# Optimization experiments

Hardware: AMD Instinct MI355X
Metric: run time of the kernel (lower is better)

## Reference

```python
import jax, jax.numpy as jnp
import numpy as np

B, H, W = 8, 256, 256
GH, GW = 32, 32          # orig_grid_shape, = img / 2^3 after three stride-2 convs
N_STEPS = 6              # masks_num: r_x_total=3, r_y_total=3, alternating dim_stride
C_FEAT = 64
N_MASK = 4               # 4 shifted supervoxel masks summed in setup
DN = ('NHWC', 'HWIO', 'NHWC')
# deconves_importances[r_x-1]; r_x sequence over steps = 1,1,2,2,3,3
LOSS_W = (0.1, 0.1, 0.5, 0.5, 1.0, 1.0)


def _conv(x, w, b, strides=(1, 1)):
    return jax.lax.conv_general_dilated(x, w, strides, 'SAME', dimension_numbers=DN) + b


def _trio(x, w, b, strides=(1, 1)):
    # Conv_trio: conv + channel norm + gelu
    y = _conv(x, w, b, strides)
    mu = jnp.mean(y, axis=-1, keepdims=True)
    var = jnp.var(y, axis=-1, keepdims=True)
    y = (y - mu) * jax.lax.rsqrt(var + 1e-6)
    return jax.nn.gelu(y)


def setup_inputs() -> dict:
    key = jax.random.key(0)
    ks = jax.random.split(key, 8)
    s = 0.05
    w1 = jax.random.normal(ks[0], (3, 3, 1, 16), jnp.float32) * s
    w2 = jax.random.normal(ks[1], (3, 3, 16, 16), jnp.float32) * s
    w3 = jax.random.normal(ks[2], (3, 3, 16, 32), jnp.float32) * s
    w4 = jax.random.normal(ks[3], (3, 3, 32, C_FEAT), jnp.float32) * s
    up_w = jax.random.normal(ks[4], (3, 3, C_FEAT, C_FEAT), jnp.float32) * s
    mask_w = jax.random.normal(ks[5], (3, 3, C_FEAT, N_MASK), jnp.float32) * s
    b1 = jnp.zeros((16,)); b2 = jnp.zeros((16,)); b3 = jnp.zeros((32,))
    b4 = jnp.zeros((C_FEAT,)); up_b = jnp.zeros((C_FEAT,)); mask_b = jnp.zeros((N_MASK,))
    # initial supervoxel masks: sum of 4 shifted checkerboards -> per-cell grid ids
    xs = jnp.arange(GH) % 2
    ys = jnp.arange(GW) % 2
    ids = (xs[:, None] + 2 * ys[None, :]).astype(jnp.float32)  # [GH,GW] in {0,1,2,3}
    masks0 = jnp.broadcast_to(ids[None, :, :, None], (B, GH, GW, 1))
    image = jax.random.normal(ks[6], (B, H, W, 1), jnp.float32)
    return {"image": image, "dynamic_cfg": 0,
            "w1": w1, "b1": b1, "w2": w2, "b2": b2, "w3": w3, "b3": b3,
            "w4": w4, "b4": b4, "up_w": up_w, "up_b": up_b,
            "mask_w": mask_w, "mask_b": mask_b, "masks0": masks0}


def reference(image, dynamic_cfg, w1, b1, w2, b2, w3, b3, w4, b4,
              up_w, up_b, mask_w, mask_b, masks0):
    # encoder: Conv_trio(16) -> (16,s2) -> (32,s2) -> (64,s2)
    x = _trio(image, w1, b1)
    x = _trio(x, w2, b2, (2, 2))
    x = _trio(x, w3, b3, (2, 2))
    deconv_multi = _trio(x, w4, b4, (2, 2))  # [B,32,32,64]
    masks = masks0
    losses = jnp.zeros((1,), image.dtype)
    offsets = jnp.arange(N_MASK, dtype=image.dtype)
    for i in range(N_STEPS):  # fixed, structurally distinct resolutions
        dim = i % 2  # alternating dim_stride as in r_x_r_y_dim_stride
        strides = (2, 1) if dim == 0 else (1, 2)
        deconv_multi = jax.nn.gelu(
            jax.lax.conv_transpose(deconv_multi, up_w, strides, 'SAME',
                                   dimension_numbers=DN) + up_b)
        probs = jax.nn.softmax(_conv(deconv_multi, mask_w, mask_b), axis=-1)  # [B,h,w,4]
        masks = jnp.repeat(masks, 2, axis=dim + 1)
        masks = masks + 0.25 * jnp.sum(probs * offsets, axis=-1, keepdims=True)
        h, w_ = deconv_multi.shape[1], deconv_multi.shape[2]
        img_ds = image.reshape(B, h, H // h, w_, W // w_, 1).mean(axis=(2, 4))
        recon = jnp.sum(probs * offsets, axis=-1, keepdims=True) / 3.0
        entropy = -jnp.sum(probs * jnp.log(probs + 1e-8), axis=-1)
        losses = losses + LOSS_W[i] * (jnp.mean(entropy) + jnp.mean((recon - img_ds) ** 2))
    return losses, masks
```

## Files before the change

### kernel.cpp

```cpp
#include <hip/hip_runtime.h>
#include <hip/hip_bf16.h>
#include <math.h>

typedef __hip_bfloat16 bf16;
typedef float f32x4 __attribute__((ext_vector_type(4)));
typedef __bf16 bf16x8 __attribute__((ext_vector_type(8)));

#define DEV __device__ __forceinline__

DEV float to_f(float v){ return v; }
DEV float to_f(bf16 v){ return __bfloat162float(v); }
DEV bf16 f2b(float v){ return __float2bfloat16(v); }
DEV unsigned short b2u(bf16 v){ return __builtin_bit_cast(unsigned short, v); }

DEV float gelu_f(float x){
  float z = 1.5957691216057308f*(x + 0.044715f*x*x*x);
  float e = __expf(-z);
  return x * __builtin_amdgcn_rcpf(1.0f + e);
}

DEV bf16x8 load_frag(const bf16* p, bool ok){
  uint4 u = make_uint4(0u,0u,0u,0u);
  if (ok) u = *(const uint4*)p;
  return __builtin_bit_cast(bf16x8, u);
}

DEV f32x4 mfma16(bf16x8 a, uint4 b, f32x4 c){
  return __builtin_amdgcn_mfma_f32_16x16x32_bf16(a, __builtin_bit_cast(bf16x8, b), c, 0, 0, 0);
}

DEV int swz8(int blk, int n){
  return (blk & 7) * (n >> 3) + (blk >> 3);
}

DEV void dma16(const void* g, void* l){
  __builtin_amdgcn_global_load_lds(
      (const __attribute__((address_space(1))) unsigned int*)g,
      (__attribute__((address_space(3))) unsigned int*)l,
      16, 0, 0);
}

#define NSLOT 64

template<typename TIN, int CIN, int COUT, int SUB, int STRIDE, int HI, int WI>
__global__ void trio_kernel(const TIN* __restrict__ in, const float* __restrict__ w,
                            const float* __restrict__ bias, bf16* __restrict__ out){
  constexpr int HO = HI/STRIDE, WO = WI/STRIDE;
  constexpr int CO_PER = COUT/SUB;
  int gtid = blockIdx.x*blockDim.x + threadIdx.x;
  int sub = gtid % SUB;
  int pix = gtid / SUB;
  int b = pix / (HO*WO); int rem = pix % (HO*WO);
  int y = rem / WO, x = rem % WO;

  float acc[CO_PER];
  #pragma unroll
  for (int j=0;j<CO_PER;j++) acc[j]=0.f;

  for (int ky=0;ky<3;ky++){
    int iy = (STRIDE==1) ? (y+ky-1) : (2*y+ky);
    if (iy<0 || iy>=HI) continue;
    for (int kx=0;kx<3;kx++){
      int ix = (STRIDE==1) ? (x+kx-1) : (2*x+kx);
      if (ix<0 || ix>=WI) continue;
      const TIN* ip = in + ((size_t)(b*HI+iy)*WI+ix)*CIN;
      const float* wp = w + ((ky*3+kx)*CIN)*COUT + sub*CO_PER;
      if constexpr (sizeof(TIN)==2 && (CIN%8)==0){
        #pragma unroll
        for (int v=0; v<CIN/8; v++){
          uint4 u = *(const uint4*)((const bf16*)ip + v*8);
          bf16x8 ch = __builtin_bit_cast(bf16x8, u);
          #pragma unroll
          for (int j=0;j<8;j++){
            float a = (float)ch[j];
            const float4* w4 = (const float4*)(wp + (size_t)(v*8+j)*COUT);
            #pragma unroll
            for (int q2=0;q2<CO_PER/4;q2++){
              float4 ww = w4[q2];
              acc[4*q2+0] += a*ww.x; acc[4*q2+1] += a*ww.y;
              acc[4*q2+2] += a*ww.z; acc[4*q2+3] += a*ww.w;
            }
          }
        }
      } else {
        #pragma unroll 4
        for (int ci=0; ci<CIN; ci++){
          float a = to_f(ip[ci]);
          const float4* w4 = (const float4*)(wp + (size_t)ci*COUT);
          #pragma unroll
          for (int j=0;j<CO_PER/4;j++){
            float4 ww = w4[j];
            acc[4*j+0] += a*ww.x; acc[4*j+1] += a*ww.y;
            acc[4*j+2] += a*ww.z; acc[4*j+3] += a*ww.w;
          }
        }
      }
    }
  }

  float s1=0.f, s2=0.f;
  #pragma unroll
  for (int j=0;j<CO_PER;j++){
    acc[j] += bias[sub*CO_PER+j];
    s1 += acc[j]; s2 += acc[j]*acc[j];
  }
  #pragma unroll
  for (int off=1; off<SUB; off<<=1){
    s1 += __shfl_xor(s1,off,64);
    s2 += __shfl_xor(s2,off,64);
  }
  float mu  = s1*(1.0f/COUT);
  float var = s2*(1.0f/COUT) - mu*mu;
  float sc  = rsqrtf(var + 1e-6f);

  bf16* op = out + (size_t)pix*COUT + sub*CO_PER;
  #pragma unroll
  for (int j=0;j<CO_PER;j++) op[j] = f2b(gelu_f((acc[j]-mu)*sc));
}

__global__ void repack_up(const float* __restrict__ w, bf16* __restrict__ bp){
  int v = blockIdx.x*256 + threadIdx.x;
  if (v >= 9*2*4*64*8) return;
  int j = v & 7; int lane = (v>>3)&63; int nt = (v>>9)&3; int c = (v>>11)&1; int tap = v>>12;
  int ci = c*32 + (lane>>4)*8 + j;
  int co = (lane&15)*4 + nt;
  bp[v] = f2b(w[(tap*64+ci)*64 + co]);
}

__global__ void repack_mask(const float* __restrict__ w, bf16* __restrict__ bp){
  int v = blockIdx.x*256 + threadIdx.x;
  if (v >= 9*2*64*8) return;
  int j = v & 7; int lane = (v>>3)&63; int c = (v>>9)&1; int tap = v>>10;
  int ci = c*32 + (lane>>4)*8 + j;
  int n = lane & 15;
  bp[v] = (n < 4) ? f2b(w[(tap*64+ci)*4 + n]) : f2b(0.0f);
}

template<int HI, int WI>
__global__ void upconv_dim0(const bf16* __restrict__ in, const bf16* __restrict__ bpack,
                            const float* __restrict__ upb, bf16* __restrict__ out){
  constexpr int HO = 2*HI, WO = WI, XT = WI/32;
  int lane = threadIdx.x & 63, wv = threadIdx.x >> 6;
  int wtile = swz8(blockIdx.x, gridDim.x)*4 + wv;
  int m = lane & 15, quad = lane >> 4;

  int x0 = (wtile % XT)*32;
  int o  = (wtile / XT) % HO;
  int b  = wtile / (XT*HO);

  int q = o >> 1;
  int stk[2], stq[2]; int nst;
  if (o & 1){ stk[0]=1; stq[0]=q; nst=1; }
  else {
    nst = 0;
    if (q >= 1){ stk[0]=0; stq[0]=q-1; nst=1; }
    stk[nst]=2; stq[nst]=q; nst++;
  }

  f32x4 acc[2][4];
  #pragma unroll
  for (int t=0;t<2;t++)
    #pragma unroll
    for (int nt=0;nt<4;nt++) acc[t][nt] = (f32x4){0.f,0.f,0.f,0.f};

  const uint4* bp4 = (const uint4*)bpack;

  #pragma unroll 1
  for (int s=0; s<nst; s++){
    int kyt = stk[s];
    const bf16* rowp = in + ((size_t)(b*HI+stq[s])*WI)*64 + quad*8;
    #pragma unroll
    for (int ut=0; ut<3; ut++){
      #pragma unroll
      for (int c=0;c<2;c++){
        int ix0 = x0 + m - 1 + ut;
        int ix1 = ix0 + 16;
        bf16x8 a0 = load_frag(rowp + (size_t)ix0*64 + c*32, ix0>=0 && ix0<WI);
        bf16x8 a1 = load_frag(rowp + (size_t)ix1*64 + c*32, ix1>=0 && ix1<WI);
        #pragma unroll
        for (int nt=0;nt<4;nt++){
          uint4 Bq = bp4[(((kyt*3+ut)*2+c)*4+nt)*64 + lane];
          acc[0][nt] = mfma16(a0, Bq, acc[0][nt]);
          acc[1][nt] = mfma16(a1, Bq, acc[1][nt]);
        }
      }
    }
  }

  float4 bv = *(const float4*)(upb + m*4);
  size_t rowbase = ((size_t)b*HO + o)*WO;
  #pragma unroll
  for (int t=0;t<2;t++){
    #pragma unroll
    for (int r=0;r<4;r++){
      int p = x0 + t*16 + quad*4 + r;
      float g0 = gelu_f(acc[t][0][r] + bv.x);
      float g1 = gelu_f(acc[t][1][r] + bv.y);
      float g2 = gelu_f(acc[t][2][r] + bv.z);
      float g3 = gelu_f(acc[t][3][r] + bv.w);
      unsigned int lo = (unsigned int)b2u(f2b(g0)) | ((unsigned int)b2u(f2b(g1))<<16);
      unsigned int hi = (unsigned int)b2u(f2b(g2)) | ((unsigned int)b2u(f2b(g3))<<16);
      *(uint2*)(out + (rowbase + p)*64 + m*4) = make_uint2(lo,hi);
    }
  }
}

template<int HI, int WI>
__global__ void __launch_bounds__(256,2)
upconv_dim0_bs(const bf16* __restrict__ in, const bf16* __restrict__ bpack,
               const float* __restrict__ upb, bf16* __restrict__ out){
  constexpr int HO = 2*HI, WO = WI, XT = WI/32;
  __shared__ __align__(16) uint4 Bsh[4608];
  int tid = threadIdx.x, lane = tid & 63, wv = tid >> 6;
  int wtile = swz8(blockIdx.x, gridDim.x)*4 + wv;
  int m = lane & 15, quad = lane >> 4;

  int x0 = (wtile % XT)*32;
  int o  = (wtile / XT) % HO;
  int b  = wtile / (XT*HO);

  {
    const uint4* gp = (const uint4*)bpack;
    #pragma unroll
    for (int k=0;k<18;k++){
      int base = (wv*18 + k)*64;
      dma16(gp + base + lane, Bsh + base);
    }
  }

  int q = o >> 1;
  int stk[2], stq[2]; int nst;
  if (o & 1){ stk[0]=1; stq[0]=q; nst=1; }
  else {
    nst = 0;
    if (q >= 1){ stk[0]=0; stq[0]=q-1; nst=1; }
    stk[nst]=2; stq[nst]=q; nst++;
  }

  f32x4 acc[2][4];
  #pragma unroll
  for (int t=0;t<2;t++)
    #pragma unroll
    for (int nt=0;nt<4;nt++) acc[t][nt] = (f32x4){0.f,0.f,0.f,0.f};

  asm volatile("s_waitcnt vmcnt(0)" ::: "memory");
  __syncthreads();

  #pragma unroll 1
  for (int s=0; s<nst; s++){
    int kyt = stk[s];
    const bf16* rowp = in + ((size_t)(b*HI+stq[s])*WI)*64 + quad*8;
    #pragma unroll
    for (int ut=0; ut<3; ut++){
      #pragma unroll
      for (int c=0;c<2;c++){
        int ix0 = x0 + m - 1 + ut;
        int ix1 = ix0 + 16;
        bf16x8 a0 = load_frag(rowp + (size_t)ix0*64 + c*32, ix0>=0 && ix0<WI);
        bf16x8 a1 = load_frag(rowp + (size_t)ix1*64 + c*32, ix1>=0 && ix1<WI);
        #pragma unroll
        for (int nt=0;nt<4;nt++){
          uint4 Bq = Bsh[(((kyt*3+ut)*2+c)*4+nt)*64 + lane];
          acc[0][nt] = mfma16(a0, Bq, acc[0][nt]);
          acc[1][nt] = mfma16(a1, Bq, acc[1][nt]);
        }
      }
    }
  }

  float4 bv = *(const float4*)(upb + m*4);
  size_t rowbase = ((size_t)b*HO + o)*WO;
  #pragma unroll
  for (int t=0;t<2;t++){
    #pragma unroll
    for (int r=0;r<4;r++){
      int p = x0 + t*16 + quad*4 + r;
      float g0 = gelu_f(acc[t][0][r] + bv.x);
      float g1 = gelu_f(acc[t][1][r] + bv.y);
      float g2 = gelu_f(acc[t][2][r] + bv.z);
      float g3 = gelu_f(acc[t][3][r] + bv.w);
      unsigned int lo = (unsigned int)b2u(f2b(g0)) | ((unsigned int)b2u(f2b(g1))<<16);
      unsigned int hi = (unsigned int)b2u(f2b(g2)) | ((unsigned int)b2u(f2b(g3))<<16);
      *(uint2*)(out + (rowbase + p)*64 + m*4) = make_uint2(lo,hi);
    }
  }
}

template<int HI, int WI>
__global__ void upconv_dim1(const bf16* __restrict__ in, const bf16* __restrict__ bpack,
                            const float* __restrict__ upb, bf16* __restrict__ out){
  constexpr int HO = HI, WO = 2*WI, QT = WI/16;
  int lane = threadIdx.x & 63, wv = threadIdx.x >> 6;
  int wtile = swz8(blockIdx.x, gridDim.x)*4 + wv;
  int m = lane & 15, quad = lane >> 4;

  int q0 = (wtile % QT)*16;
  int y  = (wtile / QT) % HI;
  int b  = wtile / (QT*HI);

  f32x4 ae[4], ao[4];
  #pragma unroll
  for (int nt=0;nt<4;nt++){ ae[nt]=(f32x4){0.f,0.f,0.f,0.f}; ao[nt]=(f32x4){0.f,0.f,0.f,0.f}; }

  const uint4* bp4 = (const uint4*)bpack;

  #pragma unroll 1
  for (int ky=0; ky<3; ky++){
    int iy = y + ky - 1;
    if (iy < 0 || iy >= HI) continue;
    const bf16* rowp = in + ((size_t)(b*HI+iy)*WI)*64 + quad*8;
    #pragma unroll
    for (int c=0;c<2;c++){
      int qa = q0 + m;
      bf16x8 Au = load_frag(rowp + (size_t)qa*64 + c*32, true);
      bf16x8 As = load_frag(rowp + (size_t)(qa-1)*64 + c*32, qa >= 1);
      #pragma unroll
      for (int nt=0;nt<4;nt++){
        uint4 B0 = bp4[(((ky*3+0)*2+c)*4+nt)*64 + lane];
        uint4 B1 = bp4[(((ky*3+1)*2+c)*4+nt)*64 + lane];
        uint4 B2 = bp4[(((ky*3+2)*2+c)*4+nt)*64 + lane];
        ae[nt] = mfma16(As, B0, ae[nt]);
        ae[nt] = mfma16(Au, B2, ae[nt]);
        ao[nt] = mfma16(Au, B1, ao[nt]);
      }
    }
  }

  float4 bv = *(const float4*)(upb + m*4);
  size_t rowbase = ((size_t)b*HO + y)*WO;
  #pragma unroll
  for (int r=0;r<4;r++){
    int qq = q0 + quad*4 + r;
    {
      float g0 = gelu_f(ae[0][r] + bv.x);
      float g1 = gelu_f(ae[1][r] + bv.y);
      float g2 = gelu_f(ae[2][r] + bv.z);
      float g3 = gelu_f(ae[3][r] + bv.w);
      unsigned int lo = (unsigned int)b2u(f2b(g0)) | ((unsigned int)b2u(f2b(g1))<<16);
      unsigned int hi = (unsigned int)b2u(f2b(g2)) | ((unsigned int)b2u(f2b(g3))<<16);
      *(uint2*)(out + (rowbase + 2*qq)*64 + m*4) = make_uint2(lo,hi);
    }
    {
      float g0 = gelu_f(ao[0][r] + bv.x);
      float g1 = gelu_f(ao[1][r] + bv.y);
      float g2 = gelu_f(ao[2][r] + bv.z);
      float g3 = gelu_f(ao[3][r] + bv.w);
      unsigned int lo = (unsigned int)b2u(f2b(g0)) | ((unsigned int)b2u(f2b(g1))<<16);
      unsigned int hi = (unsigned int)b2u(f2b(g2)) | ((unsigned int)b2u(f2b(g3))<<16);
      *(uint2*)(out + (rowbase + 2*qq+1)*64 + m*4) = make_uint2(lo,hi);
    }
  }
}

template<int HI, int WI>
__global__ void __launch_bounds__(256,2)
upconv_dim1_bs(const bf16* __restrict__ in, const bf16* __restrict__ bpack,
               const float* __restrict__ upb, bf16* __restrict__ out){
  constexpr int HO = HI, WO = 2*WI, QT = WI/16;
  __shared__ __align__(16) uint4 Bsh[4608];
  int tid = threadIdx.x, lane = tid & 63, wv = tid >> 6;
  int wtile = swz8(blockIdx.x, gridDim.x)*4 + wv;
  int m = lane & 15, quad = lane >> 4;

  int q0 = (wtile % QT)*16;
  int y  = ((wtile / QT) % (HI/2)) * 2;
  int b  = wtile / (QT*(HI/2));

  {
    const uint4* gp = (const uint4*)bpack;
    #pragma unroll
    for (int k=0;k<18;k++){
      int base = (wv*18 + k)*64;
      dma16(gp + base + lane, Bsh + base);
    }
  }

  int qa = q0 + m;

  bf16x8 Afr[4][2][2];
  #pragma unroll
  for (int i4=0;i4<4;i4++){
    int iy = y + i4 - 1;
    bool ok = (iy>=0) && (iy<HI);
    const bf16* rowp = in + ((size_t)(b*HI+iy)*WI)*64 + quad*8;
    #pragma unroll
    for (int c=0;c<2;c++){
      Afr[i4][c][0] = load_frag(rowp + (size_t)qa*64 + c*32, ok);
      Afr[i4][c][1] = load_frag(rowp + (size_t)(qa-1)*64 + c*32, ok && qa >= 1);
    }
  }

  asm volatile("s_waitcnt vmcnt(0)" ::: "memory");
  __syncthreads();

  f32x4 ae[2][4], ao[2][4];
  #pragma unroll
  for (int r=0;r<2;r++)
    #pragma unroll
    for (int nt=0;nt<4;nt++){ ae[r][nt]=(f32x4){0.f,0.f,0.f,0.f}; ao[r][nt]=(f32x4){0.f,0.f,0.f,0.f}; }

  #pragma unroll
  for (int ky=0; ky<3; ky++){
    #pragma unroll
    for (int c=0;c<2;c++){
      #pragma unroll
      for (int nt=0;nt<4;nt++){
        uint4 B0 = Bsh[(((ky*3+0)*2+c)*4+nt)*64 + lane];
        uint4 B1 = Bsh[(((ky*3+1)*2+c)*4+nt)*64 + lane];
        uint4 B2 = Bsh[(((ky*3+2)*2+c)*4+nt)*64 + lane];
        #pragma unroll
        for (int r=0;r<2;r++){
          ae[r][nt] = mfma16(Afr[ky+r][c][1], B0, ae[r][nt]);
          ae[r][nt] = mfma16(Afr[ky+r][c][0], B2, ae[r][nt]);
          ao[r][nt] = mfma16(Afr[ky+r][c][0], B1, ao[r][nt]);
        }
      }
    }
  }

  float4 bv = *(const float4*)(upb + m*4);
  #pragma unroll
  for (int r2=0;r2<2;r2++){
    size_t rowbase = ((size_t)b*HO + y + r2)*WO;
    #pragma unroll
    for (int r=0;r<4;r++){
      int qq = q0 + quad*4 + r;
      {
        float g0 = gelu_f(ae[r2][0][r] + bv.x);
        float g1 = gelu_f(ae[r2][1][r] + bv.y);
        float g2 = gelu_f(ae[r2][2][r] + bv.z);
        float g3 = gelu_f(ae[r2][3][r] + bv.w);
        unsigned int lo = (unsigned int)b2u(f2b(g0)) | ((unsigned int)b2u(f2b(g1))<<16);
        unsigned int hi = (unsigned int)b2u(f2b(g2)) | ((unsigned int)b2u(f2b(g3))<<16);
        *(uint2*)(out + (rowbase + 2*qq)*64 + m*4) = make_uint2(lo,hi);
      }
      {
        float g0 = gelu_f(ao[r2][0][r] + bv.x);
        float g1 = gelu_f(ao[r2][1][r] + bv.y);
        float g2 = gelu_f(ao[r2][2][r] + bv.z);
        float g3 = gelu_f(ao[r2][3][r] + bv.w);
        unsigned int lo = (unsigned int)b2u(f2b(g0)) | ((unsigned int)b2u(f2b(g1))<<16);
        unsigned int hi = (unsigned int)b2u(f2b(g2)) | ((unsigned int)b2u(f2b(g3))<<16);
        *(uint2*)(out + (rowbase + 2*qq+1)*64 + m*4) = make_uint2(lo,hi);
      }
    }
  }
}

template<int STEP, int DIM, int HH, int WW, int TILES>
__global__ void maskloss_mfma(const bf16* __restrict__ feat, const bf16* __restrict__ mpack,
                              const float* __restrict__ mb, const float* __restrict__ img,
                              const float* __restrict__ masks_in, float* __restrict__ masks_out,
                              float* __restrict__ accbuf){
  __shared__ float llog[4][64][4];
  __shared__ float red[4][2];
  int lane = threadIdx.x & 63;
  int wv   = threadIdx.x >> 6;
  int wtile = swz8(blockIdx.x, gridDim.x)*4 + wv;
  int m = lane & 15, quad = lane >> 4;

  constexpr int TPR = WW/(16*TILES);
  int x0 = (wtile % TPR)*(16*TILES);
  int y  = (wtile / TPR) % HH;
  int b  = wtile / (TPR*HH);

  const uint4* bp4 = (const uint4*)mpack;

  #pragma unroll 1
  for (int t=0; t<TILES; t++){
    f32x4 acc4 = (f32x4){0.f,0.f,0.f,0.f};
    #pragma unroll
    for (int c=0;c<2;c++){
      bf16x8 afr[9];
      #pragma unroll
      for (int ky=0; ky<3; ky++){
        int iy = y + ky - 1;
        bool rowok = (iy >= 0) && (iy < HH);
        const bf16* rowp = feat + ((size_t)(b*HH+iy)*WW)*64 + quad*8 + c*32;
        #pragma unroll
        for (int kx=0; kx<3; kx++){
          int ix = x0 + t*16 + m + kx - 1;
          bool ok = rowok && (ix >= 0) && (ix < WW);
          afr[ky*3+kx] = load_frag(rowp + (size_t)ix*64, ok);
        }
      }
      #pragma unroll
      for (int tap=0; tap<9; tap++){
        uint4 bb = bp4[(tap*2+c)*64 + lane];
        acc4 = mfma16(afr[tap], bb, acc4);
      }
    }
    if (m < 4){
      #pragma unroll
      for (int r=0;r<4;r++) llog[wv][t*16 + quad*4 + r][m] = acc4[r] + mb[m];
    }
  }
  __syncthreads();

  float ent = 0.f, mse = 0.f;
  if (lane < 16*TILES){
    int p = lane; int xx = x0 + p;
    float l0 = llog[wv][p][0], l1 = llog[wv][p][1];
    float l2 = llog[wv][p][2], l3 = llog[wv][p][3];
    float mx = fmaxf(fmaxf(l0,l1), fmaxf(l2,l3));
    float d0=l0-mx, d1=l1-mx, d2=l2-mx, d3=l3-mx;
    float e0=__expf(d0), e1=__expf(d1), e2=__expf(d2), e3=__expf(d3);
    float S = e0+e1+e2+e3;
    float inv = __builtin_amdgcn_rcpf(S);
    float sval = (e1 + 2.f*e2 + 3.f*e3)*inv;

    constexpr int HM = (DIM==0)? HH/2 : HH;
    constexpr int WM = (DIM==0)? WW : WW/2;
    int my = (DIM==0)? (y>>1) : y;
    int mxi = (DIM==1)? (xx>>1) : xx;
    float mv = masks_in[((size_t)b*HM + my)*WM + mxi];
    masks_out[((size_t)b*HH + y)*WW + xx] = mv + 0.25f*sval;

    ent = __logf(S) - (e0*d0 + e1*d1 + e2*d2 + e3*d3)*inv;

    constexpr int FH = 256/HH, FW = 256/WW;
    float isum = 0.f;
    const float* ib = img + ((size_t)b*256 + y*FH)*256 + xx*FW;
    #pragma unroll
    for (int dy=0; dy<FH; dy++)
      #pragma unroll
      for (int dx=0; dx<FW; dx++) isum += ib[dy*256+dx];
    float img_ds = isum * (1.0f/(FH*FW));
    float d = sval*(1.0f/3.0f) - img_ds;
    mse = d*d;
  }

  #pragma unroll
  for (int off=1; off<64; off<<=1){
    ent += __shfl_xor(ent, off, 64);
    mse += __shfl_xor(mse, off, 64);
  }
  if (lane == 0){ red[wv][0] = ent; red[wv][1] = mse; }
  __syncthreads();
  if (threadIdx.x == 0){
    float e  = red[0][0] + red[1][0] + red[2][0] + red[3][0];
    float ms = red[0][1] + red[1][1] + red[2][1] + red[3][1];
    int slot = blockIdx.x & (NSLOT-1);
    atomicAdd(accbuf + (2*STEP  )*NSLOT + slot, e);
    atomicAdd(accbuf + (2*STEP+1)*NSLOT + slot, ms);
  }
}

template<int STEP, int DIM, int HH, int WW, int ROWS>
__global__ void maskloss_lds(const bf16* __restrict__ feat, const bf16* __restrict__ mpack,
                             const float* __restrict__ mb, const float* __restrict__ img,
                             const float* __restrict__ masks_in, float* __restrict__ masks_out,
                             float* __restrict__ accbuf){
  constexpr int NBrow = WW/64;
  constexpr int PITCH = 9216;
  constexpr int NR = ROWS + 2;
  constexpr int WPR = 4/ROWS;
  __shared__ __align__(16) char smem[NR*PITCH];
  __shared__ float llog[4][ROWS][16][4];
  __shared__ float red[4][2];
  int tid = threadIdx.x;
  int lane = tid & 63, wv = tid >> 6;
  int bi = swz8(blockIdx.x, gridDim.x);
  int x0 = (bi % NBrow)*64;
  int y0 = ((bi / NBrow) % (HH/ROWS)) * ROWS;
  int b  = bi / (NBrow*(HH/ROWS));
  int m = lane & 15, quad = lane >> 4;
  int lanesw = ((lane ^ (lane>>3)) << 4);

  int r_w   = wv / WPR;
  int xbase = (wv % WPR) * (16*ROWS);
  int yw    = y0 + r_w;

  for (int k = wv; k < NR*9; k += 4){
    int r = k/9, coff = (k%9)*1024;
    int iy = y0 + r - 1;
    if (iy < 0 || iy >= HH) continue;
    const char* g = (const char*)(feat + ((size_t)(b*HH+iy)*WW + x0 - 1)*64)
                    + coff + lanesw;
    dma16(g, smem + r*PITCH + coff);
  }
  asm volatile("s_waitcnt vmcnt(0)" ::: "memory");
  __syncthreads();
  if (x0 == 0 && tid < 32*NR)
    ((float*)(smem + (tid>>5)*PITCH))[tid & 31] = 0.f;
  if (x0 + 64 == WW && tid >= 128 && tid < 128 + 32*NR){
    int t = tid - 128;
    ((float*)(smem + (t>>5)*PITCH + 65*128))[t & 31] = 0.f;
  }
  __syncthreads();

  const uint4* bp4 = (const uint4*)mpack;
  #pragma unroll
  for (int t=0; t<ROWS; t++){
    f32x4 accA = (f32x4){0.f,0.f,0.f,0.f};
    f32x4 accB = (f32x4){0.f,0.f,0.f,0.f};
    #pragma unroll
    for (int ky=0; ky<3; ky++){
      int iyw = yw + ky - 1;
      if (iyw < 0 || iyw >= HH) continue;
      const char* rowl = smem + (size_t)(r_w + ky)*PITCH;
      #pragma unroll
      for (int kx=0; kx<3; kx++){
        int lp = xbase + t*16 + m + kx;
        const char* pl = rowl + (size_t)lp*128;
        int xw = (lp & 7) << 4;
        bf16x8 a0 = __builtin_bit_cast(bf16x8, *(const uint4*)(pl + ((quad*16     ) ^ xw)));
        bf16x8 a1 = __builtin_bit_cast(bf16x8, *(const uint4*)(pl + ((quad*16 + 64) ^ xw)));
        uint4 b0 = bp4[((ky*3+kx)*2+0)*64 + lane];
        uint4 b1 = bp4[((ky*3+kx)*2+1)*64 + lane];
        accA = mfma16(a0, b0, accA);
        accB = mfma16(a1, b1, accB);
      }
    }
    if (m < 4){
      #pragma unroll
      for (int r=0;r<4;r++) llog[wv][t][quad*4+r][m] = accA[r] + accB[r] + mb[m];
    }
  }
  __syncthreads();

  float ent = 0.f, mse = 0.f;
  if (lane < 16*ROWS){
    int t = lane >> 4;
    int p = lane & 15;
    int xx = x0 + xbase + t*16 + p;
    float l0 = llog[wv][t][p][0], l1 = llog[wv][t][p][1];
    float l2 = llog[wv][t][p][2], l3 = llog[wv][t][p][3];
    float mx = fmaxf(fmaxf(l0,l1), fmaxf(l2,l3));
    float d0=l0-mx, d1=l1-mx, d2=l2-mx, d3=l3-mx;
    float e0=__expf(d0), e1=__expf(d1), e2=__expf(d2), e3=__expf(d3);
    float S = e0+e1+e2+e3;
    float inv = __builtin_amdgcn_rcpf(S);
    float sval = (e1 + 2.f*e2 + 3.f*e3)*inv;

    constexpr int HM = (DIM==0)? HH/2 : HH;
    constexpr int WM = (DIM==0)? WW : WW/2;
    int my = (DIM==0)? (yw>>1) : yw;
    int mxi = (DIM==1)? (xx>>1) : xx;
    float mv = masks_in[((size_t)b*HM + my)*WM + mxi];
    masks_out[((size_t)b*HH + yw)*WW + xx] = mv + 0.25f*sval;

    ent = __logf(S) - (e0*d0 + e1*d1 + e2*d2 + e3*d3)*inv;

    constexpr int FH = 256/HH, FW = 256/WW;
    float isum = 0.f;
    const float* ib = img + ((size_t)b*256 + yw*FH)*256 + xx*FW;
    #pragma unroll
    for (int dy=0; dy<FH; dy++)
      #pragma unroll
      for (int dx=0; dx<FW; dx++) isum += ib[dy*256+dx];
    float img_ds = isum * (1.0f/(FH*FW));
    float d = sval*(1.0f/3.0f) - img_ds;
    mse = d*d;
  }

  #pragma unroll
  for (int off=1; off<64; off<<=1){
    ent += __shfl_xor(ent, off, 64);
    mse += __shfl_xor(mse, off, 64);
  }
  if (lane == 0){ red[wv][0] = ent; red[wv][1] = mse; }
  __syncthreads();
  if (threadIdx.x == 0){
    float e  = red[0][0] + red[1][0] + red[2][0] + red[3][0];
    float ms = red[0][1] + red[1][1] + red[2][1] + red[3][1];
    int slot = blockIdx.x & (NSLOT-1);
    atomicAdd(accbuf + (2*STEP  )*NSLOT + slot, e);
    atomicAdd(accbuf + (2*STEP+1)*NSLOT + slot, ms);
  }
}

__global__ void finalize_kernel(const float* __restrict__ acc, float* __restrict__ out){
  int lane = threadIdx.x & 63;
  float v[12];
  #pragma unroll
  for (int i=0;i<12;i++){
    float x = acc[i*NSLOT + lane];
    #pragma unroll
    for (int off=1; off<64; off<<=1) x += __shfl_xor(x, off, 64);
    v[i] = x;
  }
  if (lane == 0){
    const float lw[6] = {0.1f,0.1f,0.5f,0.5f,1.0f,1.0f};
    const float nn[6] = {16384.f,32768.f,65536.f,131072.f,262144.f,524288.f};
    float L=0.f;
    for (int i=0;i<6;i++) L += lw[i]*((v[2*i] + v[2*i+1])/nn[i]);
    out[0]=L;
  }
}

extern "C" void kernel_launch(void* const* d_in, const int* in_sizes, int n_in,
                              void* d_out, int out_size, void* d_ws, size_t ws_size,
                              hipStream_t stream){
  const float* image  = (const float*)d_in[0];
  const float* w1=(const float*)d_in[2];  const float* b1=(const float*)d_in[3];
  const float* w2=(const float*)d_in[4];  const float* b2=(const float*)d_in[5];
  const float* w3=(const float*)d_in[6];  const float* b3=(const float*)d_in[7];
  const float* w4=(const float*)d_in[8];  const float* b4=(const float*)d_in[9];
  const float* upw=(const float*)d_in[10];const float* upb=(const float*)d_in[11];
  const float* mw=(const float*)d_in[12]; const float* mb=(const float*)d_in[13];
  const float* masks0=(const float*)d_in[14];
  float* out = (float*)d_out;

  char* ws = (char*)d_ws;
  size_t off = 0;
  auto alloc = [&](size_t bytes)->char*{
    char* p = ws + off; off += (bytes + 255) & ~(size_t)255; return p;
  };
  bf16* enc1  = (bf16*)alloc((size_t)8*256*256*16*2);
  bf16* enc2  = (bf16*)alloc((size_t)8*128*128*16*2);
  bf16* enc3  = (bf16*)alloc((size_t)8*64*64*32*2);
  bf16* featA = (bf16*)alloc((size_t)8*256*256*64*2);
  bf16* featB = (bf16*)alloc((size_t)8*256*128*64*2);
  float* mbA  = (float*)alloc((size_t)8*256*128*4);
  float* mbB  = (float*)alloc((size_t)8*128*128*4);
  bf16* packU = (bf16*)alloc((size_t)9*2*4*64*8*2);
  bf16* packM = (bf16*)alloc((size_t)9*2*64*8*2);
  float* acc  = (float*)alloc(12*NSLOT*sizeof(float));

  hipMemsetAsync(acc, 0, 12*NSLOT*sizeof(float), stream);

  repack_up  <<<144,256,0,stream>>>(upw, packU);
  repack_mask<<< 36,256,0,stream>>>(mw,  packM);

  trio_kernel<float,1,16,1,1,256,256><<<8*256*256/256,256,0,stream>>>(image,w1,b1,enc1);
  trio_kernel<bf16,16,16,2,2,256,256><<<8*128*128*2/256,256,0,stream>>>(enc1,w2,b2,enc2);
  trio_kernel<bf16,16,32,8,2,128,128><<<8*64*64*8/256,256,0,stream>>>(enc2,w3,b3,enc3);
  trio_kernel<bf16,32,64,16,2,64,64><<<8*32*32*16/256,256,0,stream>>>(enc3,w4,b4,featA);

  upconv_dim0<32,32><<<128,256,0,stream>>>(featA,packU,upb,featB);
  maskloss_mfma<0,0,64,32,2><<<128,256,0,stream>>>(featB,packM,mb,image,masks0,mbA,acc);
  upconv_dim1<64,32><<<256,256,0,stream>>>(featB,packU,upb,featA);
  maskloss_lds<1,1,64,64,1><<<512,256,0,stream>>>(featA,packM,mb,image,mbA,mbB,acc);
  upconv_dim0_bs<64,64><<<512,256,0,stream>>>(featA,packU,upb,featB);
  maskloss_lds<2,0,128,64,1><<<1024,256,0,stream>>>(featB,packM,mb,image,mbB,mbA,acc);
  upconv_dim1_bs<128,64><<<512,256,0,stream>>>(featB,packU,upb,featA);
  maskloss_lds<3,1,128,128,2><<<1024,256,0,stream>>>(featA,packM,mb,image,mbA,mbB,acc);
  upconv_dim0_bs<128,128><<<2048,256,0,stream>>>(featA,packU,upb,featB);
  maskloss_lds<4,0,256,128,2><<<2048,256,0,stream>>>(featB,packM,mb,image,mbB,mbA,acc);
  upconv_dim1_bs<256,128><<<2048,256,0,stream>>>(featB,packU,upb,featA);
  maskloss_lds<5,1,256,256,2><<<4096,256,0,stream>>>(featA,packM,mb,image,mbA,out+1,acc);

  finalize_kernel<<<1,64,0,stream>>>(acc,out);
}
```

Before: 403.6 us.

## Move strided encoder conv-trio layers onto MFMA with prepacked bf16 weights

```diff
diff --git a/kernel.cpp b/kernel.cpp
--- a/kernel.cpp
+++ b/kernel.cpp
@@ -65,34 +65,15 @@
       if (ix<0 || ix>=WI) continue;
       const TIN* ip = in + ((size_t)(b*HI+iy)*WI+ix)*CIN;
       const float* wp = w + ((ky*3+kx)*CIN)*COUT + sub*CO_PER;
-      if constexpr (sizeof(TIN)==2 && (CIN%8)==0){
+      #pragma unroll 4
+      for (int ci=0; ci<CIN; ci++){
+        float a = to_f(ip[ci]);
+        const float4* w4 = (const float4*)(wp + (size_t)ci*COUT);
         #pragma unroll
-        for (int v=0; v<CIN/8; v++){
-          uint4 u = *(const uint4*)((const bf16*)ip + v*8);
-          bf16x8 ch = __builtin_bit_cast(bf16x8, u);
-          #pragma unroll
-          for (int j=0;j<8;j++){
-            float a = (float)ch[j];
-            const float4* w4 = (const float4*)(wp + (size_t)(v*8+j)*COUT);
-            #pragma unroll
-            for (int q2=0;q2<CO_PER/4;q2++){
-              float4 ww = w4[q2];
-              acc[4*q2+0] += a*ww.x; acc[4*q2+1] += a*ww.y;
-              acc[4*q2+2] += a*ww.z; acc[4*q2+3] += a*ww.w;
-            }
-          }
-        }
-      } else {
-        #pragma unroll 4
-        for (int ci=0; ci<CIN; ci++){
-          float a = to_f(ip[ci]);
-          const float4* w4 = (const float4*)(wp + (size_t)ci*COUT);
-          #pragma unroll
-          for (int j=0;j<CO_PER/4;j++){
-            float4 ww = w4[j];
-            acc[4*j+0] += a*ww.x; acc[4*j+1] += a*ww.y;
-            acc[4*j+2] += a*ww.z; acc[4*j+3] += a*ww.w;
-          }
+        for (int j=0;j<CO_PER/4;j++){
+          float4 ww = w4[j];
+          acc[4*j+0] += a*ww.x; acc[4*j+1] += a*ww.y;
+          acc[4*j+2] += a*ww.z; acc[4*j+3] += a*ww.w;
         }
       }
     }
@@ -116,6 +97,111 @@
   bf16* op = out + (size_t)pix*COUT + sub*CO_PER;
   #pragma unroll
   for (int j=0;j<CO_PER;j++) op[j] = f2b(gelu_f((acc[j]-mu)*sc));
+}
+
+
+template<int COUT>
+__global__ void repack_c16(const float* __restrict__ w, bf16* __restrict__ bp){
+  constexpr int NT = COUT/16;
+  int v = blockIdx.x*256 + threadIdx.x;
+  if (v >= 5*NT*64*8) return;
+  int j = v & 7; int lane = (v>>3)&63; int idx = v>>9;
+  int nt = idx % NT; int P = idx / NT;
+  int m = lane & 15, quad = lane >> 4;
+  int tp = quad >> 1;
+  int ci = (quad & 1)*8 + j;
+  int tap = 2*P + tp;
+  int co = nt*16 + m;
+  bp[v] = (tap < 9) ? f2b(w[((size_t)tap*16 + ci)*COUT + co]) : f2b(0.0f);
+}
+
+__global__ void repack_c32(const float* __restrict__ w, bf16* __restrict__ bp){
+  int v = blockIdx.x*256 + threadIdx.x;
+  if (v >= 9*4*64*8) return;
+  int j = v & 7; int lane = (v>>3)&63; int idx = v>>9;
+  int nt = idx & 3; int tap = idx >> 2;
+  int m = lane & 15, quad = lane >> 4;
+  int ci = quad*8 + j;
+  int co = nt*16 + m;
+  bp[v] = f2b(w[((size_t)tap*32 + ci)*64 + co]);
+}
+
+template<int CIN, int COUT, int HI, int WI>
+__global__ void trio_mfma(const bf16* __restrict__ in, const bf16* __restrict__ bpack,
+                          const float* __restrict__ bias, bf16* __restrict__ out){
+  constexpr int HO = HI/2, WO = WI/2, NT = COUT/16;
+  constexpr int TPR = WO/16;
+  int lane = threadIdx.x & 63, wv = threadIdx.x >> 6;
+  int wtile = blockIdx.x*4 + wv;
+  int m = lane & 15, quad = lane >> 4;
+
+  int x0 = (wtile % TPR)*16;
+  int oy = (wtile / TPR) % HO;
+  int b  = wtile / (TPR*HO);
+
+  const uint4* bp4 = (const uint4*)bpack;
+
+  f32x4 acc[NT];
+  #pragma unroll
+  for (int nt=0;nt<NT;nt++) acc[nt] = (f32x4){0.f,0.f,0.f,0.f};
+
+  if constexpr (CIN == 32){
+    #pragma unroll
+    for (int tap=0; tap<9; tap++){
+      int ky = tap/3, kx = tap%3;
+      int iy = 2*oy + ky;
+      int ix = 2*(x0 + m) + kx;
+      bool ok = (iy < HI) && (ix < WI);
+      bf16x8 a = load_frag(in + ((size_t)(b*HI+iy)*WI + ix)*32 + quad*8, ok);
+      #pragma unroll
+      for (int nt=0;nt<NT;nt++)
+        acc[nt] = mfma16(a, bp4[(tap*NT+nt)*64 + lane], acc[nt]);
+    }
+  } else {
+    #pragma unroll
+    for (int P=0; P<5; P++){
+      int tap = 2*P + (quad >> 1);
+      int ky = tap/3, kx = tap - ky*3;
+      int iy = 2*oy + ky;
+      int ix = 2*(x0 + m) + kx;
+      bool ok = (tap < 9) && (iy < HI) && (ix < WI);
+      bf16x8 a = load_frag(in + ((size_t)(b*HI+iy)*WI + ix)*16 + (quad&1)*8, ok);
+      #pragma unroll
+      for (int nt=0;nt<NT;nt++)
+        acc[nt] = mfma16(a, bp4[(P*NT+nt)*64 + lane], acc[nt]);
+    }
+  }
+
+  float av[NT][4];
+  float s1[4] = {0.f,0.f,0.f,0.f}, s2[4] = {0.f,0.f,0.f,0.f};
+  #pragma unroll
+  for (int nt=0;nt<NT;nt++){
+    float bv = bias[nt*16 + m];
+    #pragma unroll
+    for (int r=0;r<4;r++){
+      float v = acc[nt][r] + bv;
+      av[nt][r] = v;
+      s1[r] += v; s2[r] += v*v;
+    }
+  }
+  #pragma unroll
+  for (int r=0;r<4;r++){
+    #pragma unroll
+    for (int off=1; off<16; off<<=1){
+      s1[r] += __shfl_xor(s1[r], off, 64);
+      s2[r] += __shfl_xor(s2[r], off, 64);
+    }
+  }
+  #pragma unroll
+  for (int r=0;r<4;r++){
+    float mu  = s1[r]*(1.0f/COUT);
+    float var = s2[r]*(1.0f/COUT) - mu*mu;
+    float sc  = rsqrtf(var + 1e-6f);
+    size_t px = ((size_t)(b*HO + oy))*WO + x0 + quad*4 + r;
+    #pragma unroll
+    for (int nt=0;nt<NT;nt++)
+      out[px*COUT + nt*16 + m] = f2b(gelu_f((av[nt][r]-mu)*sc));
+  }
 }
 
 __global__ void repack_up(const float* __restrict__ w, bf16* __restrict__ bp){
@@ -716,17 +802,23 @@
   float* mbB  = (float*)alloc((size_t)8*128*128*4);
   bf16* packU = (bf16*)alloc((size_t)9*2*4*64*8*2);
   bf16* packM = (bf16*)alloc((size_t)9*2*64*8*2);
+  bf16* packT2= (bf16*)alloc((size_t)5*1*64*8*2);
+  bf16* packT3= (bf16*)alloc((size_t)5*2*64*8*2);
+  bf16* packT4= (bf16*)alloc((size_t)9*4*64*8*2);
   float* acc  = (float*)alloc(12*NSLOT*sizeof(float));
 
   hipMemsetAsync(acc, 0, 12*NSLOT*sizeof(float), stream);
 
   repack_up  <<<144,256,0,stream>>>(upw, packU);
   repack_mask<<< 36,256,0,stream>>>(mw,  packM);
+  repack_c16<16><<<10,256,0,stream>>>(w2, packT2);
+  repack_c16<32><<<20,256,0,stream>>>(w3, packT3);
+  repack_c32    <<<72,256,0,stream>>>(w4, packT4);
 
   trio_kernel<float,1,16,1,1,256,256><<<8*256*256/256,256,0,stream>>>(image,w1,b1,enc1);
-  trio_kernel<bf16,16,16,2,2,256,256><<<8*128*128*2/256,256,0,stream>>>(enc1,w2,b2,enc2);
-  trio_kernel<bf16,16,32,8,2,128,128><<<8*64*64*8/256,256,0,stream>>>(enc2,w3,b3,enc3);
-  trio_kernel<bf16,32,64,16,2,64,64><<<8*32*32*16/256,256,0,stream>>>(enc3,w4,b4,featA);
+  trio_mfma<16,16,256,256><<<8*128*128/16/4,256,0,stream>>>(enc1,packT2,b2,enc2);
+  trio_mfma<16,32,128,128><<<8*64*64/16/4,256,0,stream>>>(enc2,packT3,b3,enc3);
+  trio_mfma<32,64,64,64><<<8*32*32/16/4,256,0,stream>>>(enc3,packT4,b4,featA);
 
   upconv_dim0<32,32><<<128,256,0,stream>>>(featA,packU,upb,featB);
   maskloss_mfma<0,0,64,32,2><<<128,256,0,stream>>>(featB,packM,mb,image,masks0,mbA,acc);
```

Result: faster. 351.4 us (-12.9%).
